# Optimization experiments

Hardware: AMD Instinct MI355X
Metric: run time of the kernel (lower is better)

The kernel has to match this reference:

```python
import jax, jax.numpy as jnp
import numpy as np

B, N, H, V, STEP = 16, 50, 128, 40000, 2

def setup_inputs() -> dict:
    key = jax.random.key(0)
    ks = jax.random.split(key, 24)
    def nrm(i, shape, s=0.08):
        return jax.random.normal(ks[i], shape, jnp.float32) * s
    items = jax.random.randint(ks[0], (B, N), 0, V)
    A = jax.random.uniform(ks[1], (B, N, 2 * N), jnp.float32)
    lengths = jax.random.randint(ks[2], (B,), 1, N + 1)
    mask = (jnp.arange(N)[None, :] < lengths[:, None]).astype(jnp.int32)
    emb = nrm(3, (V, H), 0.1).at[0].set(0.0)  # padding_idx=0 row zeroed
    return dict(
        items=items, A=A, mask=mask, emb=emb,
        w_ih=nrm(4, (3 * H, 2 * H)), w_hh=nrm(5, (3 * H, H)),
        b_ih=nrm(6, (3 * H,)), b_hh=nrm(7, (3 * H,)),
        b_iah=nrm(8, (H,)), b_oah=nrm(9, (H,)),
        W_ein=nrm(10, (H, H)), b_ein=nrm(11, (H,)),
        W_eout=nrm(12, (H, H)), b_eout=nrm(13, (H,)),
        W_one=nrm(14, (H, H)), b_one=nrm(15, (H,)),
        W_two=nrm(16, (H, H)), b_two=nrm(17, (H,)),
        w_three=nrm(18, (H,)),
        W_tr=nrm(19, (H, 2 * H)), b_tr=nrm(20, (H,)),
        W_t=nrm(21, (H, H)),
    )

def gnn_cell(A, hidden, w_ih, w_hh, b_ih, b_hh, b_iah, b_oah, W_ein, b_ein, W_eout, b_eout):
    # A: [B,N,2N], hidden: [B,N,H]
    ein = hidden @ W_ein.T + b_ein
    eout = hidden @ W_eout.T + b_eout
    input_in = jnp.einsum('bnm,bmh->bnh', A[:, :, :N], ein) + b_iah
    input_out = jnp.einsum('bnm,bmh->bnh', A[:, :, N:], eout) + b_oah
    inputs = jnp.concatenate([input_in, input_out], axis=-1)  # [B,N,2H]
    gi = inputs @ w_ih.T + b_ih
    gh = hidden @ w_hh.T + b_hh
    i_r, i_i, i_n = jnp.split(gi, 3, axis=-1)
    h_r, h_i, h_n = jnp.split(gh, 3, axis=-1)
    resetgate = jax.nn.sigmoid(i_r + h_r)
    inputgate = jax.nn.sigmoid(i_i + h_i)
    newgate = jnp.tanh(i_n + resetgate * h_n)
    return newgate + inputgate * (hidden - newgate)

def reference(items, A, mask, emb, w_ih, w_hh, b_ih, b_hh, b_iah, b_oah,
              W_ein, b_ein, W_eout, b_eout, W_one, b_one, W_two, b_two,
              w_three, W_tr, b_tr, W_t):
    hidden = emb[items]  # [B,N,H]
    for _ in range(STEP):
        hidden = gnn_cell(A, hidden, w_ih, w_hh, b_ih, b_hh, b_iah, b_oah,
                          W_ein, b_ein, W_eout, b_eout)
    # compute_scores
    lengths = jnp.sum(mask, axis=1)  # all >= 1 by construction
    ht = hidden[jnp.arange(B), lengths - 1]  # [B,H] last valid item
    q1 = (ht @ W_one.T + b_one)[:, None, :]
    q2 = hidden @ W_two.T + b_two
    mexp = mask[..., None].astype(jnp.float32)  # [B,N,1]
    alpha_logits = jax.nn.sigmoid(q1 + q2) @ w_three[:, None]  # [B,N,1]
    alpha = jax.nn.softmax(jnp.where(mexp == 0, -jnp.inf, alpha_logits), axis=1)
    a = jnp.sum(alpha * hidden * mexp, axis=1)  # [B,H]
    a = jnp.concatenate([a, ht], axis=1) @ W_tr.T + b_tr  # hybrid (nonhybrid=False)
    b_emb = emb[1:]  # [V-1,H]
    qt = (hidden * mexp) @ W_t.T  # [B,N,H]
    beta_logits = jnp.einsum('vh,bnh->bvn', b_emb, qt)
    beta_logits = jnp.where(mask[:, None, :] == 0, -jnp.inf, beta_logits)
    beta = jax.nn.softmax(beta_logits, axis=-1)  # [B,V-1,N]
    target = jnp.einsum('bvn,bnh->bvh', beta, qt * mexp)  # [B,V-1,H]
    # scores = sum((a[:,None,:] + target) * b_emb, -1), split to avoid extra buffer
    scores = jnp.einsum('bvh,vh->bv', target, b_emb) + a @ b_emb.T
    return scores  # [B, V-1]
```

## Files before the change

### kernel.cpp

```cpp
#include <hip/hip_runtime.h>

#define BB 16
#define NN 50
#define HH 128
#define VV 40000
#define VO 39999

typedef unsigned short u16;
typedef unsigned int u32;
typedef __attribute__((ext_vector_type(8))) short short8;
typedef __attribute__((ext_vector_type(4))) float f32x4;

#define OFF_HID    0
#define OFF_HID2   102400
#define OFF_Q2     102400
#define OFF_Q1     204800
#define OFF_HT     206848
#define OFF_WTWOT  208896
#define OFF_WTT    225280
#define OFF_WONET  241664
#define OFF_WTRT   258048
#define OFF_WEINT  290816
#define OFF_QTBF   307200
#define OFF_WEOUTT 372736
#define OFF_LEN    411648
#define OFF_WHHT   616464

__device__ __forceinline__ float sigm(float x){ return 1.0f/(1.0f+__expf(-x)); }
__device__ __forceinline__ float b2f(u16 u){
  union { u32 i; float f; } c; c.i = ((u32)u) << 16; return c.f;
}
__device__ __forceinline__ u16 f2b(float f){
  union { float f; u32 i; } c; c.f = f;
  u32 u = c.i;
  return (u16)((u + 0x7fffu + ((u >> 16) & 1u)) >> 16);
}
__device__ __forceinline__ int frag_idx(int b, int n, int k){
  int tile = n>>4, vlo = n&15, kc = k>>5, quad = (k>>3)&3, j = k&7;
  return (((b*4+tile)*4+kc)<<9) + ((quad<<4)+vlo)*8 + j;
}

__global__ void k_pre(const int* __restrict__ items, const float* __restrict__ emb,
                      const float* __restrict__ W_two, const float* __restrict__ W_t,
                      const float* __restrict__ W_one, const float* __restrict__ W_tr,
                      const float* __restrict__ W_ein, const float* __restrict__ W_eout,
                      const float* __restrict__ w_hh, float* __restrict__ ws){
  int idx = blockIdx.x*256 + threadIdx.x;
  if (idx < 102400){
    int r = idx >> 7, h = idx & 127;
    ws[OFF_HID + idx] = emb[items[r]*128 + h];
  } else if (idx < 118784){
    int i = idx-102400; int k=i>>7, h=i&127;
    ws[OFF_WTWOT + i] = W_two[h*128 + k];
  } else if (idx < 135168){
    int i = idx-118784; int k=i>>7, h=i&127;
    ws[OFF_WTT + i] = W_t[h*128 + k];
  } else if (idx < 151552){
    int i = idx-135168; int k=i>>7, h=i&127;
    ws[OFF_WONET + i] = W_one[h*128 + k];
  } else if (idx < 184320){
    int i = idx-151552; int k=i>>7, h=i&127;
    ws[OFF_WTRT + i] = W_tr[h*256 + k];
  } else if (idx < 200704){
    int i = idx-184320; int k=i>>7, h=i&127;
    ws[OFF_WEINT + i] = W_ein[h*128 + k];
  } else if (idx < 217088){
    int i = idx-200704; int k=i>>7, h=i&127;
    ws[OFF_WEOUTT + i] = W_eout[h*128 + k];
  } else if (idx < 266240){
    int i = idx-217088; int k=i/384, j=i-k*384;
    ws[OFF_WHHT + i] = w_hh[j*128 + k];
  }
}

__global__ void __launch_bounds__(512) k_step2(const float* __restrict__ A,
                       const float* __restrict__ w_ih,
                       const float* __restrict__ b_ein, const float* __restrict__ b_eout,
                       const float* __restrict__ b_iah, const float* __restrict__ b_oah,
                       const float* __restrict__ b_ih, const float* __restrict__ b_hh,
                       float* __restrict__ ws, int srcOff, int dstOff){
  __shared__ float hall[50][128];
  __shared__ float arow[4][104];
  __shared__ float ha4[4][256];
  __shared__ float sa4[4][2];
  __shared__ float inp4[4][256];
  __shared__ float gil[4][384];
  __shared__ float ghl[4][384];
  __shared__ float wtile[16][385];
  int t = threadIdx.x;
  int tile = blockIdx.x, b = blockIdx.y;
  int n0 = tile*4;
  const float* hsrc = ws + srcOff + b*6400;
  for (int o=t; o<1600; o+=512) ((float4*)hall)[o] = ((const float4*)hsrc)[o];
  if (t < 416){
    int r=t/104, c=t-r*104;
    arow[r][c] = (c<100 && n0+r<NN) ? A[(size_t)(b*NN+n0+r)*100 + c] : 0.0f;
  }
  __syncthreads();
  for (int o=t; o<1024; o+=512){
    int r = o>>8, kk = o&255;
    int k = kk & 127;
    const float* ar = &arow[r][(kk>>7)*50];
    float acc = 0.0f;
    #pragma unroll 5
    for (int m=0;m<50;m++) acc += ar[m]*hall[m][k];
    ha4[r][kk] = acc;
  }
  if (t < 8){
    int r = t>>1, half = t&1;
    const float* ar = &arow[r][half*50];
    float s = 0.0f;
    for (int m=0;m<50;m++) s += ar[m];
    sa4[r][half] = s;
  }
  __syncthreads();
  {
    int c8 = t & 255, rb = t >> 8;
    int in_half = (c8 < 128) ? 1 : 0;
    int c = c8 & 127;
    const float* wT = ws + (in_half ? OFF_WEINT : OFF_WEOUTT) + c;
    const float* haA = &ha4[rb][in_half ? 0 : 128];
    const float* haB = &ha4[rb+2][in_half ? 0 : 128];
    float a0 = in_half ? (b_iah[c] + sa4[rb  ][0]*b_ein[c]) : (b_oah[c] + sa4[rb  ][1]*b_eout[c]);
    float a1 = in_half ? (b_iah[c] + sa4[rb+2][0]*b_ein[c]) : (b_oah[c] + sa4[rb+2][1]*b_eout[c]);
    for (int k=0;k<128;k+=4){
      float w0=wT[(k+0)*128], w1=wT[(k+1)*128], w2=wT[(k+2)*128], w3=wT[(k+3)*128];
      float4 hA = *(const float4*)(haA + k);
      float4 hB = *(const float4*)(haB + k);
      a0 += hA.x*w0 + hA.y*w1 + hA.z*w2 + hA.w*w3;
      a1 += hB.x*w0 + hB.y*w1 + hB.z*w2 + hB.w*w3;
    }
    inp4[rb][c8] = a0;
    inp4[rb+2][c8] = a1;
  }
  __syncthreads();
  int j = t;
  float gacc0=0,gacc1=0,gacc2=0,gacc3=0;
  if (j < 384){ float bi = b_ih[j]; gacc0=gacc1=gacc2=gacc3=bi; }
  for (int k0=0;k0<256;k0+=16){
    #pragma unroll
    for (int q=0;q<3;q++){
      int u = t + q*512;
      int row = u>>2, seg = u&3;
      float4 v = *(const float4*)(w_ih + row*256 + k0 + seg*4);
      int kb = seg*4;
      wtile[kb+0][row]=v.x; wtile[kb+1][row]=v.y; wtile[kb+2][row]=v.z; wtile[kb+3][row]=v.w;
    }
    __syncthreads();
    if (j < 384){
      #pragma unroll
      for (int kk=0;kk<16;kk++){
        float w = wtile[kk][j];
        gacc0 += w*inp4[0][k0+kk];
        gacc1 += w*inp4[1][k0+kk];
        gacc2 += w*inp4[2][k0+kk];
        gacc3 += w*inp4[3][k0+kk];
      }
    }
    __syncthreads();
  }
  if (j < 384){ gil[0][j]=gacc0; gil[1][j]=gacc1; gil[2][j]=gacc2; gil[3][j]=gacc3; }
  if (j < 384){
    float bh = b_hh[j];
    float q0=bh,q1=bh,q2=bh,q3=bh;
    const float* wT = ws + OFF_WHHT + j;
    int r1 = (n0+1<NN)? n0+1 : n0;
    int r2 = (n0+2<NN)? n0+2 : n0;
    int r3 = (n0+3<NN)? n0+3 : n0;
    for (int k=0;k<128;k+=4){
      float w0=wT[(k+0)*384], w1=wT[(k+1)*384], w2=wT[(k+2)*384], w3=wT[(k+3)*384];
      float4 v0 = *(const float4*)(&hall[n0][k]);
      float4 v1 = *(const float4*)(&hall[r1][k]);
      float4 v2 = *(const float4*)(&hall[r2][k]);
      float4 v3 = *(const float4*)(&hall[r3][k]);
      q0 += v0.x*w0 + v0.y*w1 + v0.z*w2 + v0.w*w3;
      q1 += v1.x*w0 + v1.y*w1 + v1.z*w2 + v1.w*w3;
      q2 += v2.x*w0 + v2.y*w1 + v2.z*w2 + v2.w*w3;
      q3 += v3.x*w0 + v3.y*w1 + v3.z*w2 + v3.w*w3;
    }
    ghl[0][j]=q0; ghl[1][j]=q1; ghl[2][j]=q2; ghl[3][j]=q3;
  }
  __syncthreads();
  {
    int r = t>>7, h = t&127, row = n0+r;
    if (row < NN){
      float ir_=gil[r][h], ii=gil[r][128+h], inw=gil[r][256+h];
      float hr_=ghl[r][h], hi2=ghl[r][128+h], hn=ghl[r][256+h];
      float rg=sigm(ir_+hr_), ig=sigm(ii+hi2), ng=tanhf(inw+rg*hn);
      float hv=hall[row][h];
      ws[dstOff + (b*NN+row)*128 + h] = ng + ig*(hv-ng);
    }
  }
}

__global__ void __launch_bounds__(256) k_post(const int* __restrict__ mask,
                      const float* __restrict__ b_two, const float* __restrict__ b_one,
                      float* __restrict__ ws){
  int bx = blockIdx.x, t = threadIdx.x;
  u16* qtbf = (u16*)(ws + OFF_QTBF);
  if (bx < 200){
    bool isq2 = bx < 100;
    int r0 = (isq2 ? bx : bx-100) * 8;
    __shared__ float hl[1024];
    for (int i=0;i<4;i++) hl[t+i*256] = ws[OFF_HID + r0*128 + t + i*256];
    __syncthreads();
    int h = t & 127, g = t >> 7;
    const float* wT = ws + (isq2 ? OFF_WTWOT : OFF_WTT);
    float binit = isq2 ? b_two[h] : 0.0f;
    float acc[4];
    #pragma unroll
    for (int r=0;r<4;r++) acc[r] = binit;
    for (int k4=0;k4<32;k4++){
      int k = k4*4;
      float w0 = wT[(k+0)*128+h], w1 = wT[(k+1)*128+h];
      float w2 = wT[(k+2)*128+h], w3 = wT[(k+3)*128+h];
      #pragma unroll
      for (int r=0;r<4;r++){
        float4 hv = *(const float4*)(hl + (g*4+r)*128 + k);
        acc[r] += hv.x*w0 + hv.y*w1 + hv.z*w2 + hv.w*w3;
      }
    }
    #pragma unroll
    for (int r=0;r<4;r++){
      int row = r0 + g*4 + r;
      if (isq2) ws[OFF_Q2 + row*128 + h] = acc[r];
      else {
        float val = mask[row] ? acc[r] : 0.0f;
        int b = row/NN, n = row - b*NN;
        qtbf[frag_idx(b, n, h)] = f2b(val);
      }
    }
  } else if (bx < 248){
    int i = (bx-200)*256 + t;
    #pragma unroll
    for (int kk=0;kk<2;kk++){
      int e = i*2 + kk;
      int b = e/1536, rem = e - b*1536;
      int kc = rem/384, rem2 = rem - kc*384;
      int quad = rem2/96, vv = rem2 - quad*96;
      int vlo = 4 + vv/8, j = vv & 7;
      qtbf[(((b*4+3)*4+kc)<<9) + ((quad<<4)+vlo)*8 + j] = 0;
    }
  } else {
    __shared__ float htl[128];
    int b = bx - 248;
    if (t < 128){
      int len = 0;
      for (int n=0;n<NN;n++) len += mask[b*NN+n];
      if (len<1) len=1; if (len>NN) len=NN;
      float ht = ws[OFF_HID + (b*NN + len-1)*128 + t];
      ws[OFF_HT + b*128 + t] = ht;
      htl[t] = ht;
      if (t==0) ((int*)(ws+OFF_LEN))[b] = len;
    }
    __syncthreads();
    if (t < 128){
      const float* w1T = ws + OFF_WONET;
      float q1 = b_one[t];
      for (int k=0;k<128;k+=4){
        float4 h4v = *(const float4*)(htl + k);
        q1 += h4v.x*w1T[(k+0)*128+t] + h4v.y*w1T[(k+1)*128+t]
            + h4v.z*w1T[(k+2)*128+t] + h4v.w*w1T[(k+3)*128+t];
      }
      ws[OFF_Q1 + b*128 + t] = q1;
    }
  }
}

__global__ void __launch_bounds__(256) k_attn2(const float* __restrict__ w_three,
                        const float* __restrict__ b_tr, float* __restrict__ ws){
  __shared__ float q2l[NN*129];
  __shared__ float q1l[128], w3l[128], htl[128], al[128], pt2[128], alg[64];
  int t = threadIdx.x;
  int b = blockIdx.x;
  for (int o=t;o<6400;o+=256){ int n=o>>7, h=o&127; q2l[n*129+h] = ws[OFF_Q2 + b*6400 + o]; }
  if (t < 128){
    q1l[t] = ws[OFF_Q1 + b*128 + t];
    w3l[t] = w_three[t];
    htl[t] = ws[OFF_HT + b*128 + t];
  }
  int len = ((const int*)(ws+OFF_LEN))[b];
  __syncthreads();
  if (t < 200){
    int n = t>>2, part = t&3;
    if (n < len){
      const float* qr  = q2l + n*129 + part*32;
      const float* q1p = q1l + part*32;
      const float* w3p = w3l + part*32;
      float s = 0.0f;
      for (int h=0;h<32;h++) s += w3p[h]*sigm(q1p[h]+qr[h]);
      s += __shfl_xor(s,1); s += __shfl_xor(s,2);
      if (part==0) alg[n] = s;
    }
  }
  __syncthreads();
  if (t < 64){
    float v = (t<len) ? alg[t] : -1e30f;
    float m = v;
    m = fmaxf(m, __shfl_xor(m,1));  m = fmaxf(m, __shfl_xor(m,2));
    m = fmaxf(m, __shfl_xor(m,4));  m = fmaxf(m, __shfl_xor(m,8));
    m = fmaxf(m, __shfl_xor(m,16)); m = fmaxf(m, __shfl_xor(m,32));
    float e = (t<len) ? __expf(v - m) : 0.0f;
    float ss = e;
    ss += __shfl_xor(ss,1);  ss += __shfl_xor(ss,2);
    ss += __shfl_xor(ss,4);  ss += __shfl_xor(ss,8);
    ss += __shfl_xor(ss,16); ss += __shfl_xor(ss,32);
    float inv = 1.0f/ss;
    if (t<len) alg[t] = e*inv;
  }
  __syncthreads();
  if (t < 128){
    const float* hid = ws + OFF_HID + b*6400;
    float a = 0.0f;
    for (int n=0;n<len;n++) a += alg[n]*hid[n*128+t];
    al[t] = a;
  }
  __syncthreads();
  float p1 = 0.0f;
  if (t < 256){
    int g2 = t>>7, h = t&127;
    const float* wtr = ws + OFF_WTRT + g2*128*128;
    const float* src = g2 ? htl : al;
    float p = 0.0f;
    for (int k=0;k<128;k++) p += src[k]*wtr[k*128+h];
    if (g2) pt2[h] = p; else p1 = p;
  }
  __syncthreads();
  if (t < 128){
    float af = b_tr[t] + p1 + pt2[t];
    u16 hi = f2b(af);
    u16 lo = f2b(af - b2f(hi));
    u16* qtbf = (u16*)(ws + OFF_QTBF);
    qtbf[frag_idx(b, 50, t)] = hi;
    qtbf[frag_idx(b, 51, t)] = lo;
  }
}

__global__ void __launch_bounds__(256) k_scores(const float* __restrict__ emb,
                                                const float* __restrict__ ws,
                                                float* __restrict__ out){
  __shared__ u16 qlds[8192];
  int tid = threadIdx.x;
  int lane = tid & 63, wave = tid >> 6;
  int quad = lane >> 4, vlo = lane & 15;
  int v = blockIdx.y*64 + wave*16 + vlo;
  int vc = (v < VO) ? v : (VO-1);
  const float* erow = emb + (size_t)(vc+1)*128;
  short8 bfr[4];
  #pragma unroll
  for (int kc=0;kc<4;kc++){
    const float4* p = (const float4*)(erow + kc*32 + quad*8);
    float4 x = p[0], y = p[1];
    union { short8 s; u32 w[4]; } u;
    u.w[0] = (u32)f2b(x.x) | ((u32)f2b(x.y)<<16);
    u.w[1] = (u32)f2b(x.z) | ((u32)f2b(x.w)<<16);
    u.w[2] = (u32)f2b(y.x) | ((u32)f2b(y.y)<<16);
    u.w[3] = (u32)f2b(y.z) | ((u32)f2b(y.w)<<16);
    bfr[kc] = u.s;
  }
  const u16* qtf = (const u16*)(ws + OFF_QTBF);
  const int* slen = (const int*)(ws + OFF_LEN);
  int b0 = blockIdx.x*4;
  for (int bi=0;bi<4;bi++){
    int b = b0 + bi;
    __syncthreads();
    {
      const uint4* src = (const uint4*)qtf + (size_t)b*1024;
      uint4* dst = (uint4*)qlds;
      #pragma unroll
      for (int r=0;r<4;r++) dst[tid + r*256] = src[tid + r*256];
    }
    __syncthreads();
    int len = slen[b];
    f32x4 acc0={0.f,0.f,0.f,0.f}, acc1=acc0, acc2=acc0, acc3=acc0;
    #pragma unroll
    for (int kc=0;kc<4;kc++){
      const u16* base = qlds + kc*512 + lane*8;
      short8 a0 = *(const short8*)(base + 0*2048);
      short8 a1 = *(const short8*)(base + 1*2048);
      short8 a2 = *(const short8*)(base + 2*2048);
      short8 a3 = *(const short8*)(base + 3*2048);
      acc0 = __builtin_amdgcn_mfma_f32_16x16x32_bf16(a0, bfr[kc], acc0, 0,0,0);
      acc1 = __builtin_amdgcn_mfma_f32_16x16x32_bf16(a1, bfr[kc], acc1, 0,0,0);
      acc2 = __builtin_amdgcn_mfma_f32_16x16x32_bf16(a2, bfr[kc], acc2, 0,0,0);
      acc3 = __builtin_amdgcn_mfma_f32_16x16x32_bf16(a3, bfr[kc], acc3, 0,0,0);
    }
    int nb = quad*4;
    float ss=0.f, nm=0.f;
    #pragma unroll
    for (int r=0;r<4;r++){
      { int n=nb+r;    if(n<len){ float e=__expf(acc0[r]); ss+=e; nm+=e*acc0[r]; } }
      { int n=nb+r+16; if(n<len){ float e=__expf(acc1[r]); ss+=e; nm+=e*acc1[r]; } }
      { int n=nb+r+32; if(n<len){ float e=__expf(acc2[r]); ss+=e; nm+=e*acc2[r]; } }
      { int n=nb+r+48; if(n<len){ float e=__expf(acc3[r]); ss+=e; nm+=e*acc3[r]; } }
    }
    ss += __shfl_xor(ss,16); ss += __shfl_xor(ss,32);
    nm += __shfl_xor(nm,16); nm += __shfl_xor(nm,32);
    if (quad==0 && v < VO){
      float pa = acc3[2] + acc3[3];
      out[(size_t)b*VO + v] = nm/ss + pa;
    }
  }
}

extern "C" void kernel_launch(void* const* d_in, const int* in_sizes, int n_in,
                              void* d_out, int out_size, void* d_ws, size_t ws_size,
                              hipStream_t stream){
  const int*   items  = (const int*)d_in[0];
  const float* A      = (const float*)d_in[1];
  const int*   mask   = (const int*)d_in[2];
  const float* emb    = (const float*)d_in[3];
  const float* w_ih   = (const float*)d_in[4];
  const float* w_hh   = (const float*)d_in[5];
  const float* b_ih   = (const float*)d_in[6];
  const float* b_hh   = (const float*)d_in[7];
  const float* b_iah  = (const float*)d_in[8];
  const float* b_oah  = (const float*)d_in[9];
  const float* W_ein  = (const float*)d_in[10];
  const float* b_ein  = (const float*)d_in[11];
  const float* W_eout = (const float*)d_in[12];
  const float* b_eout = (const float*)d_in[13];
  const float* W_one  = (const float*)d_in[14];
  const float* b_one  = (const float*)d_in[15];
  const float* W_two  = (const float*)d_in[16];
  const float* b_two  = (const float*)d_in[17];
  const float* w_three= (const float*)d_in[18];
  const float* W_tr   = (const float*)d_in[19];
  const float* b_tr   = (const float*)d_in[20];
  const float* W_t    = (const float*)d_in[21];
  float* ws  = (float*)d_ws;
  float* out = (float*)d_out;

  k_pre<<<1040,256,0,stream>>>(items,emb,W_two,W_t,W_one,W_tr,W_ein,W_eout,w_hh,ws);
  k_step2<<<dim3(13,16),512,0,stream>>>(A,w_ih,b_ein,b_eout,b_iah,b_oah,b_ih,b_hh,ws,OFF_HID,OFF_HID2);
  k_step2<<<dim3(13,16),512,0,stream>>>(A,w_ih,b_ein,b_eout,b_iah,b_oah,b_ih,b_hh,ws,OFF_HID2,OFF_HID);
  k_post <<<264,256,0,stream>>>(mask,b_two,b_one,ws);
  k_attn2<<<16,256,0,stream>>>(w_three,b_tr,ws);
  k_scores<<<dim3(4,625),256,0,stream>>>(emb,ws,out);
}
```

Before: 210.6 us.

## Fuse embedding gather into first GNN step, widen w_ih tile, loop all batches in scores

The embedding gather moves out of the preprocessing kernel into the first GNN step, which reads emb rows directly into shared memory, so the hidden buffer is no longer written and re-read. The w_ih staging tile doubles from 16 to 32 k-columns, halving the number of barrier-separated iterations at the cost of more shared memory. k_scores now has each block loop over all 16 batches instead of 4, so every embedding row is converted to bf16 once instead of four times, with a quarter as many blocks. That reduces parallelism, and the first step's gather is uncoalesced per row lookup, repeated in each of 13 tile blocks.

Result: slower. 216.9 us (+3.0%).

```diff
diff --git a/kernel.cpp b/kernel.cpp
--- a/kernel.cpp
+++ b/kernel.cpp
@@ -40,45 +40,42 @@
   return (((b*4+tile)*4+kc)<<9) + ((quad<<4)+vlo)*8 + j;
 }
 
-__global__ void k_pre(const int* __restrict__ items, const float* __restrict__ emb,
-                      const float* __restrict__ W_two, const float* __restrict__ W_t,
+__global__ void k_pre(const float* __restrict__ W_two, const float* __restrict__ W_t,
                       const float* __restrict__ W_one, const float* __restrict__ W_tr,
                       const float* __restrict__ W_ein, const float* __restrict__ W_eout,
                       const float* __restrict__ w_hh, float* __restrict__ ws){
   int idx = blockIdx.x*256 + threadIdx.x;
-  if (idx < 102400){
-    int r = idx >> 7, h = idx & 127;
-    ws[OFF_HID + idx] = emb[items[r]*128 + h];
-  } else if (idx < 118784){
-    int i = idx-102400; int k=i>>7, h=i&127;
+  if (idx < 16384){
+    int i = idx; int k=i>>7, h=i&127;
     ws[OFF_WTWOT + i] = W_two[h*128 + k];
-  } else if (idx < 135168){
-    int i = idx-118784; int k=i>>7, h=i&127;
+  } else if (idx < 32768){
+    int i = idx-16384; int k=i>>7, h=i&127;
     ws[OFF_WTT + i] = W_t[h*128 + k];
-  } else if (idx < 151552){
-    int i = idx-135168; int k=i>>7, h=i&127;
+  } else if (idx < 49152){
+    int i = idx-32768; int k=i>>7, h=i&127;
     ws[OFF_WONET + i] = W_one[h*128 + k];
-  } else if (idx < 184320){
-    int i = idx-151552; int k=i>>7, h=i&127;
+  } else if (idx < 81920){
+    int i = idx-49152; int k=i>>7, h=i&127;
     ws[OFF_WTRT + i] = W_tr[h*256 + k];
-  } else if (idx < 200704){
-    int i = idx-184320; int k=i>>7, h=i&127;
+  } else if (idx < 98304){
+    int i = idx-81920; int k=i>>7, h=i&127;
     ws[OFF_WEINT + i] = W_ein[h*128 + k];
-  } else if (idx < 217088){
-    int i = idx-200704; int k=i>>7, h=i&127;
+  } else if (idx < 114688){
+    int i = idx-98304; int k=i>>7, h=i&127;
     ws[OFF_WEOUTT + i] = W_eout[h*128 + k];
-  } else if (idx < 266240){
-    int i = idx-217088; int k=i/384, j=i-k*384;
+  } else {
+    int i = idx-114688; int k=i/384, j=i-k*384;
     ws[OFF_WHHT + i] = w_hh[j*128 + k];
   }
 }
 
 __global__ void __launch_bounds__(512) k_step2(const float* __restrict__ A,
+                       const int* __restrict__ items, const float* __restrict__ emb,
                        const float* __restrict__ w_ih,
                        const float* __restrict__ b_ein, const float* __restrict__ b_eout,
                        const float* __restrict__ b_iah, const float* __restrict__ b_oah,
                        const float* __restrict__ b_ih, const float* __restrict__ b_hh,
-                       float* __restrict__ ws, int srcOff, int dstOff){
+                       float* __restrict__ ws, int srcOff, int dstOff, int firstStep){
   __shared__ float hall[50][128];
   __shared__ float arow[4][104];
   __shared__ float ha4[4][256];
@@ -86,12 +83,19 @@
   __shared__ float inp4[4][256];
   __shared__ float gil[4][384];
   __shared__ float ghl[4][384];
-  __shared__ float wtile[16][385];
+  __shared__ float wtile[32][385];
   int t = threadIdx.x;
   int tile = blockIdx.x, b = blockIdx.y;
   int n0 = tile*4;
-  const float* hsrc = ws + srcOff + b*6400;
-  for (int o=t; o<1600; o+=512) ((float4*)hall)[o] = ((const float4*)hsrc)[o];
+  if (firstStep){
+    for (int o=t; o<6400; o+=512){
+      int r=o>>7, h=o&127;
+      hall[r][h] = emb[(size_t)items[b*NN+r]*128 + h];
+    }
+  } else {
+    const float* hsrc = ws + srcOff + b*6400;
+    for (int o=t; o<1600; o+=512) ((float4*)hall)[o] = ((const float4*)hsrc)[o];
+  }
   if (t < 416){
     int r=t/104, c=t-r*104;
     arow[r][c] = (c<100 && n0+r<NN) ? A[(size_t)(b*NN+n0+r)*100 + c] : 0.0f;
@@ -137,11 +141,11 @@
   int j = t;
   float gacc0=0,gacc1=0,gacc2=0,gacc3=0;
   if (j < 384){ float bi = b_ih[j]; gacc0=gacc1=gacc2=gacc3=bi; }
-  for (int k0=0;k0<256;k0+=16){
-    #pragma unroll
-    for (int q=0;q<3;q++){
+  for (int k0=0;k0<256;k0+=32){
+    #pragma unroll
+    for (int q=0;q<6;q++){
       int u = t + q*512;
-      int row = u>>2, seg = u&3;
+      int row = u>>3, seg = u&7;
       float4 v = *(const float4*)(w_ih + row*256 + k0 + seg*4);
       int kb = seg*4;
       wtile[kb+0][row]=v.x; wtile[kb+1][row]=v.y; wtile[kb+2][row]=v.z; wtile[kb+3][row]=v.w;
@@ -149,7 +153,7 @@
     __syncthreads();
     if (j < 384){
       #pragma unroll
-      for (int kk=0;kk<16;kk++){
+      for (int kk=0;kk<32;kk++){
         float w = wtile[kk][j];
         gacc0 += w*inp4[0][k0+kk];
         gacc1 += w*inp4[1][k0+kk];
@@ -343,7 +347,7 @@
   int tid = threadIdx.x;
   int lane = tid & 63, wave = tid >> 6;
   int quad = lane >> 4, vlo = lane & 15;
-  int v = blockIdx.y*64 + wave*16 + vlo;
+  int v = blockIdx.x*64 + wave*16 + vlo;
   int vc = (v < VO) ? v : (VO-1);
   const float* erow = emb + (size_t)(vc+1)*128;
   short8 bfr[4];
@@ -360,9 +364,7 @@
   }
   const u16* qtf = (const u16*)(ws + OFF_QTBF);
   const int* slen = (const int*)(ws + OFF_LEN);
-  int b0 = blockIdx.x*4;
-  for (int bi=0;bi<4;bi++){
-    int b = b0 + bi;
+  for (int b=0;b<16;b++){
     __syncthreads();
     {
       const uint4* src = (const uint4*)qtf + (size_t)b*1024;
@@ -431,10 +433,10 @@
   float* ws  = (float*)d_ws;
   float* out = (float*)d_out;
 
-  k_pre<<<1040,256,0,stream>>>(items,emb,W_two,W_t,W_one,W_tr,W_ein,W_eout,w_hh,ws);
-  k_step2<<<dim3(13,16),512,0,stream>>>(A,w_ih,b_ein,b_eout,b_iah,b_oah,b_ih,b_hh,ws,OFF_HID,OFF_HID2);
-  k_step2<<<dim3(13,16),512,0,stream>>>(A,w_ih,b_ein,b_eout,b_iah,b_oah,b_ih,b_hh,ws,OFF_HID2,OFF_HID);
+  k_pre<<<640,256,0,stream>>>(W_two,W_t,W_one,W_tr,W_ein,W_eout,w_hh,ws);
+  k_step2<<<dim3(13,16),512,0,stream>>>(A,items,emb,w_ih,b_ein,b_eout,b_iah,b_oah,b_ih,b_hh,ws,OFF_HID,OFF_HID2,1);
+  k_step2<<<dim3(13,16),512,0,stream>>>(A,items,emb,w_ih,b_ein,b_eout,b_iah,b_oah,b_ih,b_hh,ws,OFF_HID2,OFF_HID,0);
   k_post <<<264,256,0,stream>>>(mask,b_two,b_one,ws);
   k_attn2<<<16,256,0,stream>>>(w_three,b_tr,ws);
-  k_scores<<<dim3(4,625),256,0,stream>>>(emb,ws,out);
-}
+  k_scores<<<625,256,0,stream>>>(emb,ws,out);
+}
```
